# Performance work log

Measured on AMD Instinct MI355X. Metric: run time of the kernel, lower is better.

Reference implementation:

```python
import jax, jax.numpy as jnp
import numpy as np

N, E, NNZ = 100000, 50000, 600000
D, H = 256, 8
DQH = DVH = 32
PE_DIM, HID, MAXL = 64, 256, 10
NEG = 0.2
SQRT_DQH = float(np.sqrt(DQH))


def _mlp(x, w1, b1, w2, b2):
    # 2-layer MLP (hyper_layers=2), ReLU hidden, dropout=0 at eval
    return jax.nn.relu(x @ w1 + b1) @ w2 + b2


def _ln(x, g, b, eps=1e-5):
    mu = jnp.mean(x, -1, keepdims=True)
    var = jnp.var(x, -1, keepdims=True)
    return (x - mu) * jax.lax.rsqrt(var + eps) * g + b


def _forward(x, pe_q, qw1, qb1, qw2, qb2, kw, kb, vw, vb,
             m1w1, m1b1, m1w2, m1b2, m2w1, m2b1, m2w2, m2b2,
             m3w1, m3b1, m3w2, m3b2, ln1g, ln1b, ln2g, ln2b,
             ln3g, ln3b, pe2, pe3, pe_b, bw1, bb1, bw2, bb2,
             node_idx, edge_idx, edge_orders):
    x = x + _mlp(_ln(x, ln1g, ln1b), m1w1, m1b1, m1w2, m1b2)
    # PositionalMLP queries for positions 0 and 1
    q01 = _mlp(pe_q, qw1, qb1, qw2, qb2)               # [2, H*DQH]
    q0 = q01[0].reshape(H, DQH)
    q1 = q01[1].reshape(H, DQH)
    k = x @ kw + kb                                     # [N, 2*H*DQH]
    k0 = k[:, :H * DQH].reshape(N, H, DQH)
    k1 = k[:, H * DQH:].reshape(N, H, DQH)
    v = (x @ vw + vb).reshape(N, H, DVH)
    # order-0 global attention (softmax over all N nodes)
    logit0 = jnp.einsum('hd,nhd->nh', q0, k0) / SQRT_DQH
    alpha0 = jax.nn.softmax(logit0, axis=0)
    att0 = jnp.einsum('nh,nhd->hd', alpha0, v).reshape(1, H * DVH)
    att1_v = v.reshape(N, H * DVH)
    # PMA: edge_index = incidence.indices()[[1,0]] -> source=edge_id, target=node_id
    alpha_r = jnp.sum(k1 * q1[None], -1)                # [N, H] (no sqrt scaling, as in PMA)
    a = jax.nn.leaky_relu(alpha_r[edge_idx], NEG)       # [NNZ, H]
    m = jax.ops.segment_max(a, node_idx, num_segments=N)
    a = jnp.exp(a - m[node_idx])
    s = jax.ops.segment_sum(a, node_idx, num_segments=N)
    a = a / (s[node_idx] + 1e-16)
    msg = v[edge_idx] * a[:, :, None]                   # [NNZ, H, DVH]
    att1_e = jax.ops.segment_sum(msg, node_idx, num_segments=N)[:E].reshape(E, H * DVH)

    def blk2(t, pe_row):
        h = jnp.concatenate([_ln(t, ln2g, ln2b), jnp.broadcast_to(pe_row, t.shape)], -1)
        return t + _mlp(h, m2w1, m2b1, m2w2, m2b2)

    att0 = blk2(att0, pe2[0])
    att1_v = blk2(att1_v, pe2[1])
    att1_e = blk2(att1_e, pe2[1])
    x_v = att0 + att1_v
    x_e = att0 + att1_e

    def blk3(t, pe_rows):
        h = jnp.concatenate([_ln(t, ln3g, ln3b), jnp.broadcast_to(pe_rows, t.shape)], -1)
        return t + _mlp(h, m3w1, m3b1, m3w2, m3b2)

    x_v = blk3(x_v, pe3[1])
    x_e = blk3(x_e, pe3[edge_orders])
    # BiasE: per-order bias via PositionalMLP
    bias = _mlp(pe_b, bw1, bb1, bw2, bb2)               # [MAXL+1, D]
    return x_v + bias[1], x_e + bias[edge_orders]


def setup_inputs():
    key = jax.random.key(0)
    ks = jax.random.split(key, 20)
    sc = 0.02

    def rn(i, shape):
        return jax.random.normal(ks[i], shape, jnp.float32) * sc

    def z(*sh):
        return jnp.zeros(sh, jnp.float32)

    return {
        'x': jax.random.normal(ks[0], (N, D), jnp.float32),
        'node_idx': jax.random.randint(ks[1], (NNZ,), 0, N),
        'edge_idx': jax.random.randint(ks[2], (NNZ,), 0, E),
        'edge_orders': jax.random.randint(ks[3], (E,), 0, MAXL + 1),
        'pe_q': rn(4, (2, PE_DIM)),
        'qw1': rn(5, (PE_DIM, HID)), 'qb1': z(HID),
        'qw2': rn(6, (HID, H * DQH)), 'qb2': z(H * DQH),
        'kw': rn(7, (D, 2 * H * DQH)), 'kb': z(2 * H * DQH),
        'vw': rn(8, (D, D)), 'vb': z(D),
        'm1w1': rn(9, (D, HID)), 'm1b1': z(HID), 'm1w2': rn(10, (HID, D)), 'm1b2': z(D),
        'm2w1': rn(11, (2 * D, HID)), 'm2b1': z(HID), 'm2w2': rn(12, (HID, D)), 'm2b2': z(D),
        'm3w1': rn(13, (2 * D, HID)), 'm3b1': z(HID), 'm3w2': rn(14, (HID, D)), 'm3b2': z(D),
        'ln1g': jnp.ones(D, jnp.float32), 'ln1b': z(D),
        'ln2g': jnp.ones(D, jnp.float32), 'ln2b': z(D),
        'ln3g': jnp.ones(D, jnp.float32), 'ln3b': z(D),
        'pe2': rn(15, (2, D)), 'pe3': rn(16, (MAXL + 1, D)),
        'pe_b': rn(17, (MAXL + 1, PE_DIM)),
        'bw1': rn(18, (PE_DIM, HID)), 'bb1': z(HID),
        'bw2': rn(19, (HID, D)), 'bb2': z(D),
    }


def reference(x, node_idx, edge_idx, edge_orders, pe_q, qw1, qb1, qw2, qb2,
              kw, kb, vw, vb, m1w1, m1b1, m1w2, m1b2, m2w1, m2b1, m2w2, m2b2,
              m3w1, m3b1, m3w2, m3b2, ln1g, ln1b, ln2g, ln2b, ln3g, ln3b,
              pe2, pe3, pe_b, bw1, bb1, bw2, bb2):
    return _forward(x, pe_q, qw1, qb1, qw2, qb2, kw, kb, vw, vb,
                    m1w1, m1b1, m1w2, m1b2, m2w1, m2b1, m2w2, m2b2,
                    m3w1, m3b1, m3w2, m3b2, ln1g, ln1b, ln2g, ln2b,
                    ln3g, ln3b, pe2, pe3, pe_b, bw1, bb1, bw2, bb2,
                    node_idx, edge_idx, edge_orders)
```

## Files before the change

kernel.cpp:

```cpp
#include <hip/hip_runtime.h>
#include <math.h>

#define N_NODES 100000
#define N_EDGES 50000
#define N_NNZ   600000

typedef __attribute__((ext_vector_type(8))) short bf16x8;
typedef __attribute__((ext_vector_type(4))) short bf16x4;
typedef __attribute__((ext_vector_type(4))) float f32x4;

__device__ __forceinline__ unsigned fkey(float f){
  unsigned u = __float_as_uint(f);
  return (u & 0x80000000u) ? ~u : (u | 0x80000000u);
}
__device__ __forceinline__ float fdec(unsigned k){
  return (k & 0x80000000u) ? __uint_as_float(k ^ 0x80000000u) : __uint_as_float(~k);
}
__device__ __forceinline__ short f2bf(float f){
  unsigned u = __float_as_uint(f);
  unsigned r = u + 0x7FFFu + ((u >> 16) & 1u);
  return (short)(r >> 16);
}
__device__ __forceinline__ float bf2f(short s){
  return __uint_as_float(((unsigned)(unsigned short)s) << 16);
}

__global__ void prepk(
  const float* __restrict__ ln1g, const float* __restrict__ ln1b,
  const float* __restrict__ m1w1, const float* __restrict__ m1b1,
  const float* __restrict__ ln2g, const float* __restrict__ ln2b,
  const float* __restrict__ m2w1, const float* __restrict__ m2b1,
  const float* __restrict__ ln3g, const float* __restrict__ ln3b,
  const float* __restrict__ m3w1, const float* __restrict__ m3b1,
  const float* __restrict__ pe2, const float* __restrict__ pe3,
  const float* __restrict__ pe_q, const float* __restrict__ qw1,
  const float* __restrict__ qb1, const float* __restrict__ qw2,
  const float* __restrict__ qb2, const float* __restrict__ kw,
  const float* __restrict__ kb,
  const float* __restrict__ pe_b, const float* __restrict__ bw1,
  const float* __restrict__ bb1, const float* __restrict__ bw2,
  const float* __restrict__ bb2,
  float* __restrict__ W1G1, float* __restrict__ W1G2, float* __restrict__ W1G3,
  float* __restrict__ u11, float* __restrict__ u12, float* __restrict__ u13,
  float* __restrict__ c1v, float* __restrict__ c2v, float* __restrict__ c20v,
  float* __restrict__ c3tab, float* __restrict__ kwq, float* __restrict__ kqb,
  float* __restrict__ biasT)
{
  const int b = blockIdx.x, tid = threadIdx.x;
  __shared__ float ps[11*256];
  if (b < 4) {
    for (int i = tid; i < 16384; i += 256) { int idx = b*16384 + i; W1G1[idx] = ln1g[idx>>8]*m1w1[idx]; }
  } else if (b < 8) {
    int bb = b-4;
    for (int i = tid; i < 16384; i += 256) { int idx = bb*16384 + i; W1G2[idx] = ln2g[idx>>8]*m2w1[idx]; }
  } else if (b < 12) {
    int bb = b-8;
    for (int i = tid; i < 16384; i += 256) { int idx = bb*16384 + i; W1G3[idx] = ln3g[idx>>8]*m3w1[idx]; }
  } else if (b == 12) {
    int c = tid; float su = 0.f, sc = 0.f;
    for (int k = 0; k < 256; k++) { float w = m1w1[k*256+c]; su += ln1g[k]*w; sc += ln1b[k]*w; }
    u11[c] = su; c1v[c] = m1b1[c] + sc;
  } else if (b == 13) {
    int c = tid; float su = 0.f, sl = 0.f, p0 = 0.f, p1 = 0.f;
    for (int k = 0; k < 256; k++) {
      float wl = m2w1[k*256+c], wh = m2w1[(256+k)*256+c];
      su += ln2g[k]*wl; sl += ln2b[k]*wl; p0 += pe2[k]*wh; p1 += pe2[256+k]*wh;
    }
    u12[c] = su; c2v[c] = m2b1[c] + sl + p1; c20v[c] = m2b1[c] + sl + p0;
  } else if (b == 14) {
    int c = tid; float su = 0.f, sl = 0.f;
    for (int k = 0; k < 256; k++) { float wl = m3w1[k*256+c]; su += ln3g[k]*wl; sl += ln3b[k]*wl; }
    u13[c] = su;
    float base3 = m3b1[c] + sl;
    for (int o = 0; o < 11; o++) {
      float acc = 0.f;
      for (int k = 0; k < 256; k++) acc += pe3[o*256+k]*m3w1[(256+k)*256+c];
      c3tab[o*256+c] = base3 + acc;
    }
  } else if (b == 15) {
    int j = tid;
    for (int r = 0; r < 2; r++) {
      float acc = qb1[j];
      for (int k = 0; k < 64; k++) acc += pe_q[r*64+k]*qw1[k*256+j];
      ps[r*256+j] = fmaxf(acc, 0.f);
    }
    __syncthreads();
    for (int r = 0; r < 2; r++) {
      float acc = qb2[j];
      for (int k = 0; k < 256; k++) acc += ps[r*256+k]*qw2[k*256+j];
      ps[512 + r*256 + j] = acc;
    }
    __syncthreads();
    {
      const float* q0 = &ps[512]; const float* q1 = &ps[768];
      int k = tid;
      for (int h = 0; h < 8; h++) {
        float s0 = 0.f, s1 = 0.f;
        for (int d = 0; d < 32; d++) {
          s0 += kw[k*512 + h*32 + d]       * q0[h*32+d];
          s1 += kw[k*512 + 256 + h*32 + d] * q1[h*32+d];
        }
        kwq[k*16+h]   = s0 * 0.17677669529663687f;
        kwq[k*16+8+h] = s1;
      }
      if (tid < 8) {
        float s0 = 0.f, s1 = 0.f;
        for (int d = 0; d < 32; d++) {
          s0 += kb[tid*32+d]     * q0[tid*32+d];
          s1 += kb[256+tid*32+d] * q1[tid*32+d];
        }
        kqb[tid]   = s0 * 0.17677669529663687f;
        kqb[8+tid] = s1;
      }
    }
  } else if (b == 16) {
    int j = tid;
    for (int o = 0; o < 11; o++) {
      float acc = bb1[j];
      for (int k = 0; k < 64; k++) acc += pe_b[o*64+k]*bw1[k*256+j];
      ps[o*256+j] = fmaxf(acc, 0.f);
    }
    __syncthreads();
    int c = tid;
    for (int o = 0; o < 11; o++) {
      float acc = bb2[c];
      for (int k = 0; k < 256; k++) acc += ps[o*256+k]*bw2[k*256+c];
      biasT[o*256+c] = acc;
    }
  }
}

__global__ void packk(const float* __restrict__ s0, const float* __restrict__ s1,
                      const float* __restrict__ s2, const float* __restrict__ s3,
                      const float* __restrict__ s4, const float* __restrict__ s5,
                      const float* __restrict__ s6, short* __restrict__ dst,
                      const float* __restrict__ kwq, short* __restrict__ Kqp)
{
  if (blockIdx.y == 7) {
    int k0 = blockIdx.x*32;
    int j = threadIdx.x & 15, kk = k0 + (threadIdx.x >> 4)*2;
    Kqp[j*256 + kk]   = f2bf(kwq[kk*16 + j]);
    Kqp[j*256 + kk+1] = f2bf(kwq[(kk+1)*16 + j]);
    return;
  }
  const float* srcs[7] = {s0,s1,s2,s3,s4,s5,s6};
  const float* S = srcs[blockIdx.y];
  short* D = dst + (size_t)blockIdx.y*65536;
  int n = threadIdx.x;
  int k0 = blockIdx.x*32;
  short vb[32];
  #pragma unroll
  for (int i = 0; i < 32; i++) vb[i] = f2bf(S[(k0+i)*256 + n]);
  #pragma unroll
  for (int i = 0; i < 4; i++) *(bf16x8*)&D[n*256 + k0 + i*8] = *(bf16x8*)&vb[i*8];
}

__global__ void initk(int* __restrict__ cnt, float* __restrict__ P,
                      float* __restrict__ S, unsigned* __restrict__ Mkey){
  int i = blockIdx.x*256 + threadIdx.x;
  if (i < N_EDGES) cnt[i] = 0;
  if (i < 256) P[i] = 0.f;
  if (i < 8) { S[i] = 0.f; Mkey[i] = 0u; }
}

__global__ void countk(const int* __restrict__ nidx, int* __restrict__ cnt){
  int e = blockIdx.x*256 + threadIdx.x;
  if (e < N_NNZ) { int g = nidx[e]; if (g < N_EDGES) atomicAdd(&cnt[g], 1); }
}
__global__ void scank(const int* __restrict__ cnt, int* __restrict__ offA, int* __restrict__ curA){
  __shared__ int sh[1024];
  int tid = threadIdx.x;
  const int PER = (N_EDGES + 1023)/1024;
  int base = tid*PER;
  int s = 0;
  for (int i = 0; i < PER; i++) { int idx = base+i; if (idx < N_EDGES) s += cnt[idx]; }
  sh[tid] = s;
  __syncthreads();
  for (int d = 1; d < 1024; d <<= 1) {
    int v = (tid >= d) ? sh[tid-d] : 0;
    __syncthreads();
    sh[tid] += v;
    __syncthreads();
  }
  int run = (tid == 0) ? 0 : sh[tid-1];
  for (int i = 0; i < PER; i++) {
    int idx = base+i;
    if (idx < N_EDGES) { offA[idx] = run; curA[idx] = run; run += cnt[idx]; }
  }
}
__global__ void fillk(const int* __restrict__ nidx, int* __restrict__ curA, int* __restrict__ ent){
  int e = blockIdx.x*256 + threadIdx.x;
  if (e < N_NNZ) {
    int g = nidx[e];
    if (g < N_EDGES) { int p = atomicAdd(&curA[g], 1); ent[p] = e; }
  }
}

__device__ __forceinline__ void gemm_step(const char* tb, const short* __restrict__ Wp,
    int lr, int lk, int wv, f32x4 acc[4][4])
{
  const int swzA = (lr & 7) << 4;
  const short* wb[4];
  #pragma unroll
  for (int ct = 0; ct < 4; ct++) wb[ct] = Wp + (wv*64 + ct*16 + lr)*256 + lk;
  #pragma unroll
  for (int ks = 0; ks < 8; ks++) {
    bf16x8 a[4], b[4];
    #pragma unroll
    for (int rt = 0; rt < 4; rt++)
      a[rt] = *(const bf16x8*)(tb + (((rt*16 + lr)*512 + ks*64 + lk*2) ^ swzA));
    #pragma unroll
    for (int ct = 0; ct < 4; ct++)
      b[ct] = *(const bf16x8*)(wb[ct] + ks*32);
    #pragma unroll
    for (int rt = 0; rt < 4; rt++)
      #pragma unroll
      for (int ct = 0; ct < 4; ct++)
        acc[rt][ct] = __builtin_amdgcn_mfma_f32_16x16x32_bf16(a[rt], b[ct], acc[rt][ct], 0, 0, 0);
  }
}

__device__ __forceinline__ void stats64(const char* tb, float2* red, float2* rowstat, int tid)
{
  int row = tid >> 2, q = tid & 3;
  int swz = (row & 7) << 4;
  float s = 0.f, s2 = 0.f;
  #pragma unroll
  for (int j = 0; j < 8; j++) {
    bf16x8 h = *(const bf16x8*)(tb + ((row*512 + (q*64 + j*8)*2) ^ swz));
    #pragma unroll
    for (int e = 0; e < 8; e++) { float f = bf2f(h[e]); s += f; s2 += f*f; }
  }
  red[tid] = make_float2(s, s2);
  __syncthreads();
  if (tid < 64) {
    float2 A = red[tid*4+0], B = red[tid*4+1], C = red[tid*4+2], D = red[tid*4+3];
    float ss = A.x+B.x+C.x+D.x, ss2 = A.y+B.y+C.y+D.y;
    float mu = ss * (1.f/256.f);
    float var = fmaxf(ss2*(1.f/256.f) - mu*mu, 0.f);
    rowstat[tid] = make_float2(mu, rsqrtf(var + 1e-5f));
  }
  __syncthreads();
}

__device__ __forceinline__ void epiH(char* outb, const f32x4 acc[4][4],
    const float2* rowstat, const float* __restrict__ u, const float* __restrict__ cvec,
    const int* __restrict__ cidx, int row0, int nrows, int lr, int wv, int rb)
{
  float uv[4];
  #pragma unroll
  for (int ct = 0; ct < 4; ct++) uv[ct] = u[wv*64 + ct*16 + lr];
  #pragma unroll
  for (int rt = 0; rt < 4; rt++) {
    #pragma unroll
    for (int r = 0; r < 4; r++) {
      int rl = rt*16 + rb + r;
      float2 st = rowstat[rl];
      const float* cb = cvec;
      if (cidx != nullptr) {
        int gr = row0 + rl;
        cb = cvec + (size_t)((gr < nrows) ? cidx[gr] : 0)*256;
      }
      int swz = (rl & 7) << 4;
      #pragma unroll
      for (int ct = 0; ct < 4; ct++) {
        int j = wv*64 + ct*16 + lr;
        float h = fmaxf(st.y*(acc[rt][ct][r] - st.x*uv[ct]) + cb[j], 0.f);
        *(short*)(outb + ((rl*512 + j*2) ^ swz)) = f2bf(h);
      }
    }
  }
}

__global__ __launch_bounds__(256, 2) void fusedAk(
  const float* __restrict__ x,
  const short* __restrict__ Wp1, const float* __restrict__ u1, const float* __restrict__ c1,
  const short* __restrict__ Wp2, const float* __restrict__ b2,
  const short* __restrict__ Wpv, const float* __restrict__ vb,
  const short* __restrict__ Kqp, const float* __restrict__ kqb,
  short* __restrict__ vout, float* __restrict__ lb, int nrows)
{
  __shared__ __align__(16) short bufA[64*256];
  __shared__ __align__(16) short bufB[64*256];
  __shared__ float2 red[256];
  __shared__ float2 rowstat[64];
  char* tA = (char*)bufA; char* tB = (char*)bufB;
  const int tid = threadIdx.x;
  const int wv = tid >> 6, lane = tid & 63;
  const int lr = lane & 15, lk = (lane >> 4)*8, rb = (lane >> 4)*4;
  const int row0 = blockIdx.x * 64;

  {
    int row = tid >> 2, c0 = (tid & 3)*64;
    bool ok = (row0 + row < nrows);
    const float* sp = x + (size_t)(row0+row)*256 + c0;
    int swz = (row & 7) << 4;
    #pragma unroll
    for (int j = 0; j < 8; j++) {
      float4 f0 = ok ? *(const float4*)(sp + j*8)     : make_float4(0,0,0,0);
      float4 f1 = ok ? *(const float4*)(sp + j*8 + 4) : make_float4(0,0,0,0);
      bf16x8 h;
      h[0]=f2bf(f0.x); h[1]=f2bf(f0.y); h[2]=f2bf(f0.z); h[3]=f2bf(f0.w);
      h[4]=f2bf(f1.x); h[5]=f2bf(f1.y); h[6]=f2bf(f1.z); h[7]=f2bf(f1.w);
      *(bf16x8*)(tA + ((row*512 + (c0+j*8)*2) ^ swz)) = h;
    }
  }
  __syncthreads();
  stats64(tA, red, rowstat, tid);

  const f32x4 zero = {0.f,0.f,0.f,0.f};
  f32x4 acc[4][4];
  #pragma unroll
  for (int rt = 0; rt < 4; rt++)
    #pragma unroll
    for (int ct = 0; ct < 4; ct++) acc[rt][ct] = zero;
  gemm_step(tA, Wp1, lr, lk, wv, acc);
  epiH(tB, acc, rowstat, u1, c1, nullptr, row0, nrows, lr, wv, rb);
  __syncthreads();

  #pragma unroll
  for (int rt = 0; rt < 4; rt++)
    #pragma unroll
    for (int ct = 0; ct < 4; ct++) acc[rt][ct] = zero;
  gemm_step(tB, Wp2, lr, lk, wv, acc);
  {
    float bv[4];
    #pragma unroll
    for (int ct = 0; ct < 4; ct++) bv[ct] = b2[wv*64 + ct*16 + lr];
    #pragma unroll
    for (int rt = 0; rt < 4; rt++) {
      #pragma unroll
      for (int r = 0; r < 4; r++) {
        int rl = rt*16 + rb + r;
        int gr = row0 + rl;
        bool ok = gr < nrows;
        const float* xp = x + (size_t)gr*256;
        int swz = (rl & 7) << 4;
        #pragma unroll
        for (int ct = 0; ct < 4; ct++) {
          int j = wv*64 + ct*16 + lr;
          float xv = ok ? xp[j] : 0.f;
          float x1 = xv + acc[rt][ct][r] + bv[ct];
          *(short*)(tA + ((rl*512 + j*2) ^ swz)) = f2bf(x1);
        }
      }
    }
  }
  __syncthreads();

  #pragma unroll
  for (int rt = 0; rt < 4; rt++)
    #pragma unroll
    for (int ct = 0; ct < 4; ct++) acc[rt][ct] = zero;
  gemm_step(tA, Wpv, lr, lk, wv, acc);
  {
    float bv[4];
    #pragma unroll
    for (int ct = 0; ct < 4; ct++) bv[ct] = vb[wv*64 + ct*16 + lr];
    #pragma unroll
    for (int rt = 0; rt < 4; rt++) {
      #pragma unroll
      for (int r = 0; r < 4; r++) {
        int rl = rt*16 + rb + r;
        int gr = row0 + rl;
        if (gr >= nrows) continue;
        #pragma unroll
        for (int ct = 0; ct < 4; ct++) {
          int j = wv*64 + ct*16 + lr;
          vout[(size_t)gr*256 + j] = f2bf(acc[rt][ct][r] + bv[ct]);
        }
      }
    }
  }
  {
    f32x4 aq = zero;
    int arow = wv*16 + lr;
    int swzq = (lr & 7) << 4;
    #pragma unroll
    for (int ks = 0; ks < 8; ks++) {
      bf16x8 a = *(const bf16x8*)(tA + ((arow*512 + ks*64 + lk*2) ^ swzq));
      bf16x8 b = *(const bf16x8*)(Kqp + lr*256 + ks*32 + lk);
      aq = __builtin_amdgcn_mfma_f32_16x16x32_bf16(a, b, aq, 0, 0, 0);
    }
    float kq = kqb[lr];
    #pragma unroll
    for (int r = 0; r < 4; r++) {
      int gr = row0 + wv*16 + rb + r;
      if (gr < nrows) lb[gr*16 + lr] = aq[r] + kq;
    }
  }
}

__global__ __launch_bounds__(256, 2) void fused2k(
  const short* __restrict__ srcb, float* __restrict__ dst, int nrows,
  const short* __restrict__ Wp21, const float* __restrict__ u2, const float* __restrict__ c2,
  const short* __restrict__ Wp22, const float* __restrict__ b22, const float* __restrict__ add2,
  const short* __restrict__ Wp31, const float* __restrict__ u3, const float* __restrict__ c3, const int* __restrict__ c3idx,
  const short* __restrict__ Wp32, const float* __restrict__ b32, const float* __restrict__ add3, const int* __restrict__ a3idx)
{
  __shared__ __align__(16) short bufA[64*256];
  __shared__ __align__(16) short bufB[64*256];
  __shared__ float2 red[256];
  __shared__ float2 rowstat[64];
  char* tA = (char*)bufA; char* tB = (char*)bufB;
  const int tid = threadIdx.x;
  const int wv = tid >> 6, lane = tid & 63;
  const int lr = lane & 15, lk = (lane >> 4)*8, rb = (lane >> 4)*4;
  const int row0 = blockIdx.x * 64;

  {
    int row = tid >> 2, c0 = (tid & 3)*64;
    bool ok = (row0 + row < nrows);
    const short* sp = srcb + (size_t)(row0+row)*256 + c0;
    int swz = (row & 7) << 4;
    const bf16x8 zz = {0,0,0,0,0,0,0,0};
    #pragma unroll
    for (int j = 0; j < 8; j++) {
      bf16x8 h = ok ? *(const bf16x8*)(sp + j*8) : zz;
      *(bf16x8*)(tA + ((row*512 + (c0+j*8)*2) ^ swz)) = h;
    }
  }
  __syncthreads();
  stats64(tA, red, rowstat, tid);

  const f32x4 zero = {0.f,0.f,0.f,0.f};
  f32x4 acc[4][4];
  #pragma unroll
  for (int rt = 0; rt < 4; rt++)
    #pragma unroll
    for (int ct = 0; ct < 4; ct++) acc[rt][ct] = zero;
  gemm_step(tA, Wp21, lr, lk, wv, acc);
  epiH(tB, acc, rowstat, u2, c2, nullptr, row0, nrows, lr, wv, rb);
  __syncthreads();

  #pragma unroll
  for (int rt = 0; rt < 4; rt++)
    #pragma unroll
    for (int ct = 0; ct < 4; ct++) acc[rt][ct] = zero;
  gemm_step(tB, Wp22, lr, lk, wv, acc);

  float t2r[4][4][4];
  {
    float bv[4], av[4];
    #pragma unroll
    for (int ct = 0; ct < 4; ct++) {
      int j = wv*64 + ct*16 + lr;
      bv[ct] = b22[j]; av[ct] = add2[j];
    }
    #pragma unroll
    for (int rt = 0; rt < 4; rt++) {
      #pragma unroll
      for (int r = 0; r < 4; r++) {
        int rl = rt*16 + rb + r;
        int swz = (rl & 7) << 4;
        #pragma unroll
        for (int ct = 0; ct < 4; ct++) {
          int j = wv*64 + ct*16 + lr;
          float vres = bf2f(*(const short*)(tA + ((rl*512 + j*2) ^ swz)));
          float t2 = vres + acc[rt][ct][r] + bv[ct] + av[ct];
          t2r[rt][ct][r] = t2;
          *(short*)(tA + ((rl*512 + j*2) ^ swz)) = f2bf(t2);
        }
      }
    }
  }
  __syncthreads();
  stats64(tA, red, rowstat, tid);

  #pragma unroll
  for (int rt = 0; rt < 4; rt++)
    #pragma unroll
    for (int ct = 0; ct < 4; ct++) acc[rt][ct] = zero;
  gemm_step(tA, Wp31, lr, lk, wv, acc);
  epiH(tB, acc, rowstat, u3, c3, c3idx, row0, nrows, lr, wv, rb);
  __syncthreads();

  #pragma unroll
  for (int rt = 0; rt < 4; rt++)
    #pragma unroll
    for (int ct = 0; ct < 4; ct++) acc[rt][ct] = zero;
  gemm_step(tB, Wp32, lr, lk, wv, acc);

  {
    float bv[4];
    #pragma unroll
    for (int ct = 0; ct < 4; ct++) bv[ct] = b32[wv*64 + ct*16 + lr];
    #pragma unroll
    for (int rt = 0; rt < 4; rt++) {
      #pragma unroll
      for (int r = 0; r < 4; r++) {
        int rl = rt*16 + rb + r;
        int gr = row0 + rl;
        if (gr >= nrows) continue;
        const float* ap = add3 + (size_t)((a3idx != nullptr) ? a3idx[gr] : 0)*256;
        #pragma unroll
        for (int ct = 0; ct < 4; ct++) {
          int j = wv*64 + ct*16 + lr;
          dst[(size_t)gr*256 + j] = t2r[rt][ct][r] + acc[rt][ct][r] + bv[ct] + ap[j];
        }
      }
    }
  }
}

__global__ void maxk(const float* __restrict__ lb, unsigned* __restrict__ Mkey){
  float mx[8];
  #pragma unroll
  for (int h = 0; h < 8; h++) mx[h] = -INFINITY;
  for (int n = blockIdx.x*256 + threadIdx.x; n < N_NODES; n += 65536) {
    float4 a = *(const float4*)&lb[n*16];
    float4 b = *(const float4*)&lb[n*16+4];
    mx[0] = fmaxf(mx[0], a.x); mx[1] = fmaxf(mx[1], a.y);
    mx[2] = fmaxf(mx[2], a.z); mx[3] = fmaxf(mx[3], a.w);
    mx[4] = fmaxf(mx[4], b.x); mx[5] = fmaxf(mx[5], b.y);
    mx[6] = fmaxf(mx[6], b.z); mx[7] = fmaxf(mx[7], b.w);
  }
  __shared__ unsigned bm[8];
  if (threadIdx.x < 8) bm[threadIdx.x] = 0u;
  __syncthreads();
  #pragma unroll
  for (int h = 0; h < 8; h++) atomicMax(&bm[h], fkey(mx[h]));
  __syncthreads();
  if (threadIdx.x < 8) atomicMax(&Mkey[threadIdx.x], bm[threadIdx.x]);
}

__global__ void sumk(const float* __restrict__ lb, const short* __restrict__ v,
                     const unsigned* __restrict__ Mkey,
                     float* __restrict__ P, float* __restrict__ S)
{
  int tid = threadIdx.x; int h = tid >> 5;
  float Mh = fdec(Mkey[h]);
  float pa = 0.f, sa = 0.f;
  for (int n = blockIdx.x; n < N_NODES; n += gridDim.x) {
    float w = expf(lb[n*16 + h] - Mh);
    pa = fmaf(w, bf2f(v[(size_t)n*256 + tid]), pa);
    sa += w;
  }
  atomicAdd(&P[tid], pa);
  if ((tid & 31) == 0) atomicAdd(&S[h], sa);
}

__global__ __launch_bounds__(256) void aggk(
  const int* __restrict__ offA, const int* __restrict__ cnt,
  const int* __restrict__ ent, const int* __restrict__ eidx,
  const float* __restrict__ lb, const short* __restrict__ v,
  short* __restrict__ out)
{
  int g = blockIdx.x*4 + (threadIdx.x >> 6);
  if (g >= N_EDGES) return;
  int lane = threadIdx.x & 63;
  int h = lane >> 3;
  int co = lane*4;
  int base = offA[g], n = cnt[g];
  float m = -INFINITY, s = 0.f;
  float ax = 0.f, ay = 0.f, az = 0.f, aw = 0.f;
  for (int i = 0; i < n; i++) {
    int src = eidx[ent[base + i]];
    float ar = lb[src*16 + 8 + h];
    float a = (ar > 0.f) ? ar : 0.2f*ar;
    float mn = fmaxf(m, a);
    float sc = expf(m - mn);
    float p  = expf(a - mn);
    s = s*sc + p;
    bf16x4 vv = *(const bf16x4*)(v + (size_t)src*256 + co);
    ax = ax*sc + p*bf2f(vv[0]); ay = ay*sc + p*bf2f(vv[1]);
    az = az*sc + p*bf2f(vv[2]); aw = aw*sc + p*bf2f(vv[3]);
    m = mn;
  }
  float inv = 1.f/(s + 1e-16f);
  bf16x4 o4;
  o4[0] = f2bf(ax*inv); o4[1] = f2bf(ay*inv);
  o4[2] = f2bf(az*inv); o4[3] = f2bf(aw*inv);
  *(bf16x4*)(out + (size_t)g*256 + co) = o4;
}

__global__ void att0k(const float* __restrict__ P, const float* __restrict__ S,
                      const float* __restrict__ c20, const float* __restrict__ W1G2,
                      const float* __restrict__ m2w2, const float* __restrict__ m2b2,
                      float* __restrict__ att0b)
{
  __shared__ float a0[256], zs[256], Hs[256];
  __shared__ float part[4];
  __shared__ float stat[2];
  int c = threadIdx.x;
  float av = P[c] / S[c >> 5];
  a0[c] = av;
  float x = av;
  for (int o = 32; o > 0; o >>= 1) x += __shfl_down(x, o);
  if ((c & 63) == 0) part[c >> 6] = x;
  __syncthreads();
  if (c == 0) stat[0] = (part[0]+part[1]+part[2]+part[3])*(1.f/256.f);
  __syncthreads();
  float mu = stat[0];
  float d = av - mu;
  x = d*d;
  for (int o = 32; o > 0; o >>= 1) x += __shfl_down(x, o);
  if ((c & 63) == 0) part[c >> 6] = x;
  __syncthreads();
  if (c == 0) stat[1] = rsqrtf((part[0]+part[1]+part[2]+part[3])*(1.f/256.f) + 1e-5f);
  __syncthreads();
  zs[c] = (av - mu)*stat[1];
  __syncthreads();
  float acc = c20[c];
  for (int k = 0; k < 256; k++) acc = fmaf(zs[k], W1G2[k*256 + c], acc);
  Hs[c] = fmaxf(acc, 0.f);
  __syncthreads();
  float acc2 = m2b2[c];
  for (int k = 0; k < 256; k++) acc2 = fmaf(Hs[k], m2w2[k*256 + c], acc2);
  att0b[c] = a0[c] + acc2;
}

extern "C" void kernel_launch(void* const* d_in, const int* in_sizes, int n_in,
                              void* d_out, int out_size, void* d_ws, size_t ws_size,
                              hipStream_t stream)
{
  const float* x    = (const float*)d_in[0];
  const int*   nidx = (const int*)d_in[1];
  const int*   eidx = (const int*)d_in[2];
  const int*   eord = (const int*)d_in[3];
  const float* pe_q = (const float*)d_in[4];
  const float* qw1  = (const float*)d_in[5];
  const float* qb1  = (const float*)d_in[6];
  const float* qw2  = (const float*)d_in[7];
  const float* qb2  = (const float*)d_in[8];
  const float* kw   = (const float*)d_in[9];
  const float* kb   = (const float*)d_in[10];
  const float* vw   = (const float*)d_in[11];
  const float* vb   = (const float*)d_in[12];
  const float* m1w1 = (const float*)d_in[13];
  const float* m1b1 = (const float*)d_in[14];
  const float* m1w2 = (const float*)d_in[15];
  const float* m1b2 = (const float*)d_in[16];
  const float* m2w1 = (const float*)d_in[17];
  const float* m2b1 = (const float*)d_in[18];
  const float* m2w2 = (const float*)d_in[19];
  const float* m2b2 = (const float*)d_in[20];
  const float* m3w1 = (const float*)d_in[21];
  const float* m3b1 = (const float*)d_in[22];
  const float* m3w2 = (const float*)d_in[23];
  const float* m3b2 = (const float*)d_in[24];
  const float* ln1g = (const float*)d_in[25];
  const float* ln1b = (const float*)d_in[26];
  const float* ln2g = (const float*)d_in[27];
  const float* ln2b = (const float*)d_in[28];
  const float* ln3g = (const float*)d_in[29];
  const float* ln3b = (const float*)d_in[30];
  const float* pe2  = (const float*)d_in[31];
  const float* pe3  = (const float*)d_in[32];
  const float* pe_b = (const float*)d_in[33];
  const float* bw1  = (const float*)d_in[34];
  const float* bb1  = (const float*)d_in[35];
  const float* bw2  = (const float*)d_in[36];
  const float* bb2  = (const float*)d_in[37];

  float* out_v = (float*)d_out;
  float* out_e = out_v + (size_t)N_NODES*256;

  float* ws = (float*)d_ws;
  size_t o = 0;
  short* vbf  = (short*)(ws + o); o += (size_t)N_NODES*128;
  short* aeb  = (short*)(ws + o); o += (size_t)N_EDGES*128;
  float* lb    = ws + o; o += (size_t)N_NODES*16;
  float* W1G1  = ws + o; o += 65536;
  float* W1G2  = ws + o; o += 65536;
  float* W1G3  = ws + o; o += 65536;
  float* kwq   = ws + o; o += 4096;
  float* kqb   = ws + o; o += 256;
  float* biasT = ws + o; o += 11*256;
  float* u11   = ws + o; o += 256;
  float* u12   = ws + o; o += 256;
  float* u13   = ws + o; o += 256;
  float* c1v   = ws + o; o += 256;
  float* c2v   = ws + o; o += 256;
  float* c20v  = ws + o; o += 256;
  float* c3tab = ws + o; o += 11*256;
  float* att0b = ws + o; o += 256;
  float* Pacc  = ws + o; o += 256;
  float* Sacc  = ws + o; o += 256;
  unsigned* Mkey = (unsigned*)(ws + o); o += 256;
  int* cnt  = (int*)(ws + o); o += N_EDGES;
  int* offA = (int*)(ws + o); o += N_EDGES;
  int* curA = (int*)(ws + o); o += N_EDGES;
  int* ent  = (int*)(ws + o); o += N_NNZ;
  short* Wpall = (short*)(ws + o); o += 7*32768;
  short* Kqp   = (short*)(ws + o); o += 2048;
  (void)in_sizes; (void)n_in; (void)out_size; (void)ws_size;

  short* Wp_w1g1 = Wpall + 0*65536;
  short* Wp_w1g2 = Wpall + 1*65536;
  short* Wp_w1g3 = Wpall + 2*65536;
  short* Wp_m1w2 = Wpall + 3*65536;
  short* Wp_m2w2 = Wpall + 4*65536;
  short* Wp_m3w2 = Wpall + 5*65536;
  short* Wp_vw   = Wpall + 6*65536;

  const int GN = (N_NODES + 63)/64;
  const int GE = (N_EDGES + 63)/64;

  prepk<<<17, 256, 0, stream>>>(ln1g, ln1b, m1w1, m1b1, ln2g, ln2b, m2w1, m2b1,
                                ln3g, ln3b, m3w1, m3b1, pe2, pe3,
                                pe_q, qw1, qb1, qw2, qb2, kw, kb,
                                pe_b, bw1, bb1, bw2, bb2,
                                W1G1, W1G2, W1G3, u11, u12, u13,
                                c1v, c2v, c20v, c3tab, kwq, kqb, biasT);
  packk<<<dim3(8, 8), 256, 0, stream>>>(W1G1, W1G2, W1G3, m1w2, m2w2, m3w2, vw, Wpall, kwq, Kqp);
  initk<<<196, 256, 0, stream>>>(cnt, Pacc, Sacc, Mkey);
  countk<<<(N_NNZ + 255)/256, 256, 0, stream>>>(nidx, cnt);

  fusedAk<<<GN, 256, 0, stream>>>(x, Wp_w1g1, u11, c1v, Wp_m1w2, m1b2,
                                  Wp_vw, vb, Kqp, kqb, vbf, lb, N_NODES);

  maxk<<<256, 256, 0, stream>>>(lb, Mkey);
  sumk<<<1024, 256, 0, stream>>>(lb, vbf, Mkey, Pacc, Sacc);

  scank<<<1, 1024, 0, stream>>>(cnt, offA, curA);
  fillk<<<(N_NNZ + 255)/256, 256, 0, stream>>>(nidx, curA, ent);
  aggk<<<N_EDGES/4, 256, 0, stream>>>(offA, cnt, ent, eidx, lb, vbf, aeb);

  att0k<<<1, 256, 0, stream>>>(Pacc, Sacc, c20v, W1G2, m2w2, m2b2, att0b);

  fused2k<<<GN, 256, 0, stream>>>(vbf, out_v, N_NODES,
                                  Wp_w1g2, u12, c2v, Wp_m2w2, m2b2, att0b,
                                  Wp_w1g3, u13, c3tab + 256, nullptr,
                                  Wp_m3w2, m3b2, biasT + 256, nullptr);
  fused2k<<<GE, 256, 0, stream>>>(aeb, out_e, N_EDGES,
                                  Wp_w1g2, u12, c2v, Wp_m2w2, m2b2, att0b,
                                  Wp_w1g3, u13, c3tab, eord,
                                  Wp_m3w2, m3b2, biasT, eord);
}
```

Before: 1.231 ms.

## Widen fused MLP kernels to 8 waves and stage outputs through LDS

The fused row-MLP kernels move from 4 waves to 8 waves per 64-row tile, so each wave computes 32 output columns instead of 64. This halves the accumulator registers per thread and should allow more waves in flight to hide LDS and weight-load latency. Output stores for v and the final float result are now staged through shared memory and written as coalesced 16-byte vectors instead of scattered scalar stores. The cost is extra LDS round-trips and barriers, and each B-fragment now feeds fewer MFMAs, lowering register-level reuse of the weights.

```diff
diff --git a/kernel.cpp b/kernel.cpp
--- a/kernel.cpp
+++ b/kernel.cpp
@@ -196,46 +196,51 @@
   }
 }
 
-__device__ __forceinline__ void gemm_step(const char* tb, const short* __restrict__ Wp,
-    int lr, int lk, int wv, f32x4 acc[4][4])
+__device__ __forceinline__ void gemm8(const char* tb, const short* __restrict__ Wp,
+    int lr, int lk, int wv, f32x4 acc[4][2])
 {
   const int swzA = (lr & 7) << 4;
-  const short* wb[4];
-  #pragma unroll
-  for (int ct = 0; ct < 4; ct++) wb[ct] = Wp + (wv*64 + ct*16 + lr)*256 + lk;
+  const short* w0 = Wp + (size_t)(wv*32 + lr)*256 + lk;
+  const short* w1 = w0 + 16*256;
   #pragma unroll
   for (int ks = 0; ks < 8; ks++) {
-    bf16x8 a[4], b[4];
+    bf16x8 a[4];
     #pragma unroll
     for (int rt = 0; rt < 4; rt++)
       a[rt] = *(const bf16x8*)(tb + (((rt*16 + lr)*512 + ks*64 + lk*2) ^ swzA));
-    #pragma unroll
-    for (int ct = 0; ct < 4; ct++)
-      b[ct] = *(const bf16x8*)(wb[ct] + ks*32);
-    #pragma unroll
-    for (int rt = 0; rt < 4; rt++)
-      #pragma unroll
-      for (int ct = 0; ct < 4; ct++)
-        acc[rt][ct] = __builtin_amdgcn_mfma_f32_16x16x32_bf16(a[rt], b[ct], acc[rt][ct], 0, 0, 0);
-  }
-}
-
-__device__ __forceinline__ void stats64(const char* tb, float2* red, float2* rowstat, int tid)
-{
-  int row = tid >> 2, q = tid & 3;
+    bf16x8 b0 = *(const bf16x8*)(w0 + ks*32);
+    bf16x8 b1 = *(const bf16x8*)(w1 + ks*32);
+    #pragma unroll
+    for (int rt = 0; rt < 4; rt++) {
+      acc[rt][0] = __builtin_amdgcn_mfma_f32_16x16x32_bf16(a[rt], b0, acc[rt][0], 0, 0, 0);
+      acc[rt][1] = __builtin_amdgcn_mfma_f32_16x16x32_bf16(a[rt], b1, acc[rt][1], 0, 0, 0);
+    }
+  }
+}
+
+__device__ __forceinline__ void zacc(f32x4 acc[4][2]){
+  const f32x4 z = {0.f,0.f,0.f,0.f};
+  #pragma unroll
+  for (int rt = 0; rt < 4; rt++) { acc[rt][0] = z; acc[rt][1] = z; }
+}
+
+__device__ __forceinline__ void stats512(const char* tb, float2* red, float2* rowstat, int tid)
+{
+  int row = tid >> 3, q = tid & 7;
   int swz = (row & 7) << 4;
   float s = 0.f, s2 = 0.f;
   #pragma unroll
-  for (int j = 0; j < 8; j++) {
-    bf16x8 h = *(const bf16x8*)(tb + ((row*512 + (q*64 + j*8)*2) ^ swz));
+  for (int j = 0; j < 4; j++) {
+    bf16x8 h = *(const bf16x8*)(tb + ((row*512 + (q*32 + j*8)*2) ^ swz));
     #pragma unroll
     for (int e = 0; e < 8; e++) { float f = bf2f(h[e]); s += f; s2 += f*f; }
   }
   red[tid] = make_float2(s, s2);
   __syncthreads();
   if (tid < 64) {
-    float2 A = red[tid*4+0], B = red[tid*4+1], C = red[tid*4+2], D = red[tid*4+3];
-    float ss = A.x+B.x+C.x+D.x, ss2 = A.y+B.y+C.y+D.y;
+    float ss = 0.f, ss2 = 0.f;
+    #pragma unroll
+    for (int k = 0; k < 8; k++) { float2 p = red[tid*8+k]; ss += p.x; ss2 += p.y; }
     float mu = ss * (1.f/256.f);
     float var = fmaxf(ss2*(1.f/256.f) - mu*mu, 0.f);
     rowstat[tid] = make_float2(mu, rsqrtf(var + 1e-5f));
@@ -243,13 +248,12 @@
   __syncthreads();
 }
 
-__device__ __forceinline__ void epiH(char* outb, const f32x4 acc[4][4],
+__device__ __forceinline__ void epiH512(char* outb, const f32x4 acc[4][2],
     const float2* rowstat, const float* __restrict__ u, const float* __restrict__ cvec,
     const int* __restrict__ cidx, int row0, int nrows, int lr, int wv, int rb)
 {
-  float uv[4];
-  #pragma unroll
-  for (int ct = 0; ct < 4; ct++) uv[ct] = u[wv*64 + ct*16 + lr];
+  float uv0 = u[wv*32 + lr], uv1 = u[wv*32 + 16 + lr];
+  const int j0 = wv*32 + lr, j1 = j0 + 16;
   #pragma unroll
   for (int rt = 0; rt < 4; rt++) {
     #pragma unroll
@@ -262,17 +266,15 @@
         cb = cvec + (size_t)((gr < nrows) ? cidx[gr] : 0)*256;
       }
       int swz = (rl & 7) << 4;
-      #pragma unroll
-      for (int ct = 0; ct < 4; ct++) {
-        int j = wv*64 + ct*16 + lr;
-        float h = fmaxf(st.y*(acc[rt][ct][r] - st.x*uv[ct]) + cb[j], 0.f);
-        *(short*)(outb + ((rl*512 + j*2) ^ swz)) = f2bf(h);
-      }
-    }
-  }
-}
-
-__global__ __launch_bounds__(256, 2) void fusedAk(
+      float h0 = fmaxf(st.y*(acc[rt][0][r] - st.x*uv0) + cb[j0], 0.f);
+      float h1 = fmaxf(st.y*(acc[rt][1][r] - st.x*uv1) + cb[j1], 0.f);
+      *(short*)(outb + ((rl*512 + j0*2) ^ swz)) = f2bf(h0);
+      *(short*)(outb + ((rl*512 + j1*2) ^ swz)) = f2bf(h1);
+    }
+  }
+}
+
+__global__ __launch_bounds__(512, 4) void fusedAk(
   const float* __restrict__ x,
   const short* __restrict__ Wp1, const float* __restrict__ u1, const float* __restrict__ c1,
   const short* __restrict__ Wp2, const float* __restrict__ b2,
@@ -280,23 +282,24 @@
   const short* __restrict__ Kqp, const float* __restrict__ kqb,
   short* __restrict__ vout, float* __restrict__ lb, int nrows)
 {
-  __shared__ __align__(16) short bufA[64*256];
-  __shared__ __align__(16) short bufB[64*256];
-  __shared__ float2 red[256];
+  __shared__ __align__(16) char smem[65536];
+  __shared__ float2 red[512];
   __shared__ float2 rowstat[64];
-  char* tA = (char*)bufA; char* tB = (char*)bufB;
+  char* tA = smem;
+  char* tB = smem + 32768;
   const int tid = threadIdx.x;
   const int wv = tid >> 6, lane = tid & 63;
   const int lr = lane & 15, lk = (lane >> 4)*8, rb = (lane >> 4)*4;
   const int row0 = blockIdx.x * 64;
+  const int j0 = wv*32 + lr, j1 = j0 + 16;
 
   {
-    int row = tid >> 2, c0 = (tid & 3)*64;
+    int row = tid >> 3, c0 = (tid & 7)*32;
     bool ok = (row0 + row < nrows);
     const float* sp = x + (size_t)(row0+row)*256 + c0;
     int swz = (row & 7) << 4;
     #pragma unroll
-    for (int j = 0; j < 8; j++) {
+    for (int j = 0; j < 4; j++) {
       float4 f0 = ok ? *(const float4*)(sp + j*8)     : make_float4(0,0,0,0);
       float4 f1 = ok ? *(const float4*)(sp + j*8 + 4) : make_float4(0,0,0,0);
       bf16x8 h;
@@ -306,27 +309,18 @@
     }
   }
   __syncthreads();
-  stats64(tA, red, rowstat, tid);
-
-  const f32x4 zero = {0.f,0.f,0.f,0.f};
-  f32x4 acc[4][4];
-  #pragma unroll
-  for (int rt = 0; rt < 4; rt++)
-    #pragma unroll
-    for (int ct = 0; ct < 4; ct++) acc[rt][ct] = zero;
-  gemm_step(tA, Wp1, lr, lk, wv, acc);
-  epiH(tB, acc, rowstat, u1, c1, nullptr, row0, nrows, lr, wv, rb);
-  __syncthreads();
-
-  #pragma unroll
-  for (int rt = 0; rt < 4; rt++)
-    #pragma unroll
-    for (int ct = 0; ct < 4; ct++) acc[rt][ct] = zero;
-  gemm_step(tB, Wp2, lr, lk, wv, acc);
+  stats512(tA, red, rowstat, tid);
+
+  f32x4 acc[4][2];
+  zacc(acc);
+  gemm8(tA, Wp1, lr, lk, wv, acc);
+  epiH512(tB, acc, rowstat, u1, c1, nullptr, row0, nrows, lr, wv, rb);
+  __syncthreads();
+
+  zacc(acc);
+  gemm8(tB, Wp2, lr, lk, wv, acc);
   {
-    float bv[4];
-    #pragma unroll
-    for (int ct = 0; ct < 4; ct++) bv[ct] = b2[wv*64 + ct*16 + lr];
+    float bv0 = b2[j0], bv1 = b2[j1];
     #pragma unroll
     for (int rt = 0; rt < 4; rt++) {
       #pragma unroll
@@ -336,169 +330,160 @@
         bool ok = gr < nrows;
         const float* xp = x + (size_t)gr*256;
         int swz = (rl & 7) << 4;
-        #pragma unroll
-        for (int ct = 0; ct < 4; ct++) {
-          int j = wv*64 + ct*16 + lr;
-          float xv = ok ? xp[j] : 0.f;
-          float x1 = xv + acc[rt][ct][r] + bv[ct];
-          *(short*)(tA + ((rl*512 + j*2) ^ swz)) = f2bf(x1);
-        }
+        float x0 = ok ? xp[j0] : 0.f;
+        float x1v = ok ? xp[j1] : 0.f;
+        *(short*)(tA + ((rl*512 + j0*2) ^ swz)) = f2bf(x0 + acc[rt][0][r] + bv0);
+        *(short*)(tA + ((rl*512 + j1*2) ^ swz)) = f2bf(x1v + acc[rt][1][r] + bv1);
       }
     }
   }
   __syncthreads();
 
-  #pragma unroll
-  for (int rt = 0; rt < 4; rt++)
-    #pragma unroll
-    for (int ct = 0; ct < 4; ct++) acc[rt][ct] = zero;
-  gemm_step(tA, Wpv, lr, lk, wv, acc);
+  zacc(acc);
+  gemm8(tA, Wpv, lr, lk, wv, acc);
+
+  f32x4 aq = {0.f,0.f,0.f,0.f};
+  if (wv < 4) {
+    int arow = wv*16 + lr;
+    int swzq = (lr & 7) << 4;
+    #pragma unroll
+    for (int ks = 0; ks < 8; ks++) {
+      bf16x8 a = *(const bf16x8*)(tA + ((arow*512 + ks*64 + lk*2) ^ swzq));
+      bf16x8 b = *(const bf16x8*)(Kqp + lr*256 + ks*32 + lk);
+      aq = __builtin_amdgcn_mfma_f32_16x16x32_bf16(a, b, aq, 0, 0, 0);
+    }
+  }
+
   {
-    float bv[4];
-    #pragma unroll
-    for (int ct = 0; ct < 4; ct++) bv[ct] = vb[wv*64 + ct*16 + lr];
+    float vb0 = vb[j0], vb1 = vb[j1];
+    short* tv = (short*)tB;
+    #pragma unroll
+    for (int rt = 0; rt < 4; rt++) {
+      #pragma unroll
+      for (int r = 0; r < 4; r++) {
+        int rl = rt*16 + rb + r;
+        tv[rl*256 + j0] = f2bf(acc[rt][0][r] + vb0);
+        tv[rl*256 + j1] = f2bf(acc[rt][1][r] + vb1);
+      }
+    }
+  }
+  __syncthreads();
+  {
+    const short* tv = (const short*)tB;
+    #pragma unroll
+    for (int i = 0; i < 4; i++) {
+      int s = i*512 + tid;
+      int row = s >> 5, gr = row0 + row;
+      if (gr < nrows)
+        *(bf16x8*)&vout[(size_t)gr*256 + (s & 31)*8] = *(const bf16x8*)&tv[(size_t)s*8];
+    }
+  }
+  if (wv < 4) {
+    float kq = kqb[lr];
+    #pragma unroll
+    for (int r = 0; r < 4; r++) {
+      int gr = row0 + wv*16 + rb + r;
+      if (gr < nrows) lb[(size_t)gr*16 + lr] = aq[r] + kq;
+    }
+  }
+}
+
+__global__ __launch_bounds__(512, 4) void fused2k(
+  const short* __restrict__ srcb, float* __restrict__ dst, int nrows,
+  const short* __restrict__ Wp21, const float* __restrict__ u2, const float* __restrict__ c2,
+  const short* __restrict__ Wp22, const float* __restrict__ b22, const float* __restrict__ add2,
+  const short* __restrict__ Wp31, const float* __restrict__ u3, const float* __restrict__ c3, const int* __restrict__ c3idx,
+  const short* __restrict__ Wp32, const float* __restrict__ b32, const float* __restrict__ add3, const int* __restrict__ a3idx)
+{
+  __shared__ __align__(16) char smem[65536];
+  __shared__ float2 red[512];
+  __shared__ float2 rowstat[64];
+  char* tA = smem;
+  char* tB = smem + 32768;
+  const int tid = threadIdx.x;
+  const int wv = tid >> 6, lane = tid & 63;
+  const int lr = lane & 15, lk = (lane >> 4)*8, rb = (lane >> 4)*4;
+  const int row0 = blockIdx.x * 64;
+  const int j0 = wv*32 + lr, j1 = j0 + 16;
+
+  {
+    int row = tid >> 3, c0 = (tid & 7)*32;
+    bool ok = (row0 + row < nrows);
+    const short* sp = srcb + (size_t)(row0+row)*256 + c0;
+    int swz = (row & 7) << 4;
+    const bf16x8 zz = {0,0,0,0,0,0,0,0};
+    #pragma unroll
+    for (int j = 0; j < 4; j++) {
+      bf16x8 h = ok ? *(const bf16x8*)(sp + j*8) : zz;
+      *(bf16x8*)(tA + ((row*512 + (c0+j*8)*2) ^ swz)) = h;
+    }
+  }
+  __syncthreads();
+  stats512(tA, red, rowstat, tid);
+
+  f32x4 acc[4][2];
+  zacc(acc);
+  gemm8(tA, Wp21, lr, lk, wv, acc);
+  epiH512(tB, acc, rowstat, u2, c2, nullptr, row0, nrows, lr, wv, rb);
+  __syncthreads();
+
+  zacc(acc);
+  gemm8(tB, Wp22, lr, lk, wv, acc);
+
+  f32x4 t2a[4], t2b[4];
+  {
+    float bv0 = b22[j0], bv1 = b22[j1];
+    float av0 = add2[j0], av1 = add2[j1];
+    #pragma unroll
+    for (int rt = 0; rt < 4; rt++) {
+      #pragma unroll
+      for (int r = 0; r < 4; r++) {
+        int rl = rt*16 + rb + r;
+        int swz = (rl & 7) << 4;
+        float v0 = bf2f(*(const short*)(tA + ((rl*512 + j0*2) ^ swz)));
+        float v1 = bf2f(*(const short*)(tA + ((rl*512 + j1*2) ^ swz)));
+        float t0 = v0 + acc[rt][0][r] + bv0 + av0;
+        float t1 = v1 + acc[rt][1][r] + bv1 + av1;
+        t2a[rt][r] = t0; t2b[rt][r] = t1;
+        *(short*)(tA + ((rl*512 + j0*2) ^ swz)) = f2bf(t0);
+        *(short*)(tA + ((rl*512 + j1*2) ^ swz)) = f2bf(t1);
+      }
+    }
+  }
+  __syncthreads();
+  stats512(tA, red, rowstat, tid);
+
+  zacc(acc);
+  gemm8(tA, Wp31, lr, lk, wv, acc);
+  epiH512(tB, acc, rowstat, u3, c3, c3idx, row0, nrows, lr, wv, rb);
+  __syncthreads();
+
+  zacc(acc);
+  gemm8(tB, Wp32, lr, lk, wv, acc);
+  __syncthreads();
+
+  {
+    float* smemF = (float*)smem;
+    float bv0 = b32[j0], bv1 = b32[j1];
     #pragma unroll
     for (int rt = 0; rt < 4; rt++) {
       #pragma unroll
       for (int r = 0; r < 4; r++) {
         int rl = rt*16 + rb + r;
         int gr = row0 + rl;
-        if (gr >= nrows) continue;
-        #pragma unroll
-        for (int ct = 0; ct < 4; ct++) {
-          int j = wv*64 + ct*16 + lr;
-          vout[(size_t)gr*256 + j] = f2bf(acc[rt][ct][r] + bv[ct]);
-        }
+        int ai = (a3idx != nullptr && gr < nrows) ? a3idx[gr] : 0;
+        const float* ap = add3 + (size_t)ai*256;
+        smemF[rl*256 + j0] = t2a[rt][r] + acc[rt][0][r] + bv0 + ap[j0];
+        smemF[rl*256 + j1] = t2b[rt][r] + acc[rt][1][r] + bv1 + ap[j1];
       }
     }
-  }
-  {
-    f32x4 aq = zero;
-    int arow = wv*16 + lr;
-    int swzq = (lr & 7) << 4;
-    #pragma unroll
-    for (int ks = 0; ks < 8; ks++) {
-      bf16x8 a = *(const bf16x8*)(tA + ((arow*512 + ks*64 + lk*2) ^ swzq));
-      bf16x8 b = *(const bf16x8*)(Kqp + lr*256 + ks*32 + lk);
-      aq = __builtin_amdgcn_mfma_f32_16x16x32_bf16(a, b, aq, 0, 0, 0);
-    }
-    float kq = kqb[lr];
-    #pragma unroll
-    for (int r = 0; r < 4; r++) {
-      int gr = row0 + wv*16 + rb + r;
-      if (gr < nrows) lb[gr*16 + lr] = aq[r] + kq;
-    }
-  }
-}
-
-__global__ __launch_bounds__(256, 2) void fused2k(
-  const short* __restrict__ srcb, float* __restrict__ dst, int nrows,
-  const short* __restrict__ Wp21, const float* __restrict__ u2, const float* __restrict__ c2,
-  const short* __restrict__ Wp22, const float* __restrict__ b22, const float* __restrict__ add2,
-  const short* __restrict__ Wp31, const float* __restrict__ u3, const float* __restrict__ c3, const int* __restrict__ c3idx,
-  const short* __restrict__ Wp32, const float* __restrict__ b32, const float* __restrict__ add3, const int* __restrict__ a3idx)
-{
-  __shared__ __align__(16) short bufA[64*256];
-  __shared__ __align__(16) short bufB[64*256];
-  __shared__ float2 red[256];
-  __shared__ float2 rowstat[64];
-  char* tA = (char*)bufA; char* tB = (char*)bufB;
-  const int tid = threadIdx.x;
-  const int wv = tid >> 6, lane = tid & 63;
-  const int lr = lane & 15, lk = (lane >> 4)*8, rb = (lane >> 4)*4;
-  const int row0 = blockIdx.x * 64;
-
-  {
-    int row = tid >> 2, c0 = (tid & 3)*64;
-    bool ok = (row0 + row < nrows);
-    const short* sp = srcb + (size_t)(row0+row)*256 + c0;
-    int swz = (row & 7) << 4;
-    const bf16x8 zz = {0,0,0,0,0,0,0,0};
-    #pragma unroll
-    for (int j = 0; j < 8; j++) {
-      bf16x8 h = ok ? *(const bf16x8*)(sp + j*8) : zz;
-      *(bf16x8*)(tA + ((row*512 + (c0+j*8)*2) ^ swz)) = h;
-    }
-  }
-  __syncthreads();
-  stats64(tA, red, rowstat, tid);
-
-  const f32x4 zero = {0.f,0.f,0.f,0.f};
-  f32x4 acc[4][4];
-  #pragma unroll
-  for (int rt = 0; rt < 4; rt++)
-    #pragma unroll
-    for (int ct = 0; ct < 4; ct++) acc[rt][ct] = zero;
-  gemm_step(tA, Wp21, lr, lk, wv, acc);
-  epiH(tB, acc, rowstat, u2, c2, nullptr, row0, nrows, lr, wv, rb);
-  __syncthreads();
-
-  #pragma unroll
-  for (int rt = 0; rt < 4; rt++)
-    #pragma unroll
-    for (int ct = 0; ct < 4; ct++) acc[rt][ct] = zero;
-  gemm_step(tB, Wp22, lr, lk, wv, acc);
-
-  float t2r[4][4][4];
-  {
-    float bv[4], av[4];
-    #pragma unroll
-    for (int ct = 0; ct < 4; ct++) {
-      int j = wv*64 + ct*16 + lr;
-      bv[ct] = b22[j]; av[ct] = add2[j];
-    }
-    #pragma unroll
-    for (int rt = 0; rt < 4; rt++) {
-      #pragma unroll
-      for (int r = 0; r < 4; r++) {
-        int rl = rt*16 + rb + r;
-        int swz = (rl & 7) << 4;
-        #pragma unroll
-        for (int ct = 0; ct < 4; ct++) {
-          int j = wv*64 + ct*16 + lr;
-          float vres = bf2f(*(const short*)(tA + ((rl*512 + j*2) ^ swz)));
-          float t2 = vres + acc[rt][ct][r] + bv[ct] + av[ct];
-          t2r[rt][ct][r] = t2;
-          *(short*)(tA + ((rl*512 + j*2) ^ swz)) = f2bf(t2);
-        }
-      }
-    }
-  }
-  __syncthreads();
-  stats64(tA, red, rowstat, tid);
-
-  #pragma unroll
-  for (int rt = 0; rt < 4; rt++)
-    #pragma unroll
-    for (int ct = 0; ct < 4; ct++) acc[rt][ct] = zero;
-  gemm_step(tA, Wp31, lr, lk, wv, acc);
-  epiH(tB, acc, rowstat, u3, c3, c3idx, row0, nrows, lr, wv, rb);
-  __syncthreads();
-
-  #pragma unroll
-  for (int rt = 0; rt < 4; rt++)
-    #pragma unroll
-    for (int ct = 0; ct < 4; ct++) acc[rt][ct] = zero;
-  gemm_step(tB, Wp32, lr, lk, wv, acc);
-
-  {
-    float bv[4];
-    #pragma unroll
-    for (int ct = 0; ct < 4; ct++) bv[ct] = b32[wv*64 + ct*16 + lr];
-    #pragma unroll
-    for (int rt = 0; rt < 4; rt++) {
-      #pragma unroll
-      for (int r = 0; r < 4; r++) {
-        int rl = rt*16 + rb + r;
-        int gr = row0 + rl;
-        if (gr >= nrows) continue;
-        const float* ap = add3 + (size_t)((a3idx != nullptr) ? a3idx[gr] : 0)*256;
-        #pragma unroll
-        for (int ct = 0; ct < 4; ct++) {
-          int j = wv*64 + ct*16 + lr;
-          dst[(size_t)gr*256 + j] = t2r[rt][ct][r] + acc[rt][ct][r] + bv[ct] + ap[j];
-        }
-      }
+    __syncthreads();
+    #pragma unroll
+    for (int i = 0; i < 8; i++) {
+      int s = i*512 + tid;
+      int row = s >> 6, gr = row0 + row;
+      if (gr < nrows)
+        *(float4*)&dst[(size_t)gr*256 + (s & 63)*4] = *(const float4*)&smemF[(size_t)s*4];
     }
   }
 }
@@ -707,7 +692,7 @@
   initk<<<196, 256, 0, stream>>>(cnt, Pacc, Sacc, Mkey);
   countk<<<(N_NNZ + 255)/256, 256, 0, stream>>>(nidx, cnt);
 
-  fusedAk<<<GN, 256, 0, stream>>>(x, Wp_w1g1, u11, c1v, Wp_m1w2, m1b2,
+  fusedAk<<<GN, 512, 0, stream>>>(x, Wp_w1g1, u11, c1v, Wp_m1w2, m1b2,
                                   Wp_vw, vb, Kqp, kqb, vbf, lb, N_NODES);
 
   maxk<<<256, 256, 0, stream>>>(lb, Mkey);
@@ -719,11 +704,11 @@
 
   att0k<<<1, 256, 0, stream>>>(Pacc, Sacc, c20v, W1G2, m2w2, m2b2, att0b);
 
-  fused2k<<<GN, 256, 0, stream>>>(vbf, out_v, N_NODES,
+  fused2k<<<GN, 512, 0, stream>>>(vbf, out_v, N_NODES,
                                   Wp_w1g2, u12, c2v, Wp_m2w2, m2b2, att0b,
                                   Wp_w1g3, u13, c3tab + 256, nullptr,
                                   Wp_m3w2, m3b2, biasT + 256, nullptr);
-  fused2k<<<GE, 256, 0, stream>>>(aeb, out_e, N_EDGES,
+  fused2k<<<GE, 512, 0, stream>>>(aeb, out_e, N_EDGES,
                                   Wp_w1g2, u12, c2v, Wp_m2w2, m2b2, att0b,
                                   Wp_w1g3, u13, c3tab, eord,
                                   Wp_m3w2, m3b2, biasT, eord);
```

Result: faster. 1.200 ms (-2.5%).
